# Kernel tuning notes

Hardware: AMD Instinct MI355X
Metric: run time of the kernel (lower is better)

## Reference

```python
import jax, jax.numpy as jnp
import numpy as np

B, T, CIN = 32, 4096, 165
CH, RCH, EDIM, NEMB = 256, 32, 64, 512


def setup_inputs() -> dict:
    key = jax.random.key(0)
    ks = iter(jax.random.split(key, 40))

    def w(o, i):
        return jax.random.normal(next(ks), (o, i), jnp.float32) * (1.0 / np.sqrt(i))

    def b(o):
        return jnp.zeros((o,), jnp.float32)

    inp = {"x": jax.random.normal(next(ks), (B, T, CIN), jnp.float32)}
    # Encoder: conv(165->128), relu, conv(128->256), relu, conv(256->256), 2 resblocks, relu
    inp["enc_w0"], inp["enc_b0"] = w(CH // 2, CIN), b(CH // 2)
    inp["enc_w1"], inp["enc_b1"] = w(CH, CH // 2), b(CH)
    inp["enc_w2"], inp["enc_b2"] = w(CH, CH), b(CH)
    inp["er0_w0"], inp["er0_b0"] = w(RCH, CH), b(RCH)
    inp["er0_w1"], inp["er0_b1"] = w(CH, RCH), b(CH)
    inp["er1_w0"], inp["er1_b0"] = w(RCH, CH), b(RCH)
    inp["er1_w1"], inp["er1_b1"] = w(CH, RCH), b(CH)
    # quantize_conv (256->64)
    inp["qc_w"], inp["qc_b"] = w(EDIM, CH), b(EDIM)
    # codebook [dim, n_embed]
    inp["embed"] = jax.random.normal(next(ks), (EDIM, NEMB), jnp.float32)
    # Decoder: conv(64->256), 2 resblocks, relu, conv(256->128), relu, conv(128->165)
    inp["dec_w0"], inp["dec_b0"] = w(CH, EDIM), b(CH)
    inp["dr0_w0"], inp["dr0_b0"] = w(RCH, CH), b(RCH)
    inp["dr0_w1"], inp["dr0_b1"] = w(CH, RCH), b(CH)
    inp["dr1_w0"], inp["dr1_b0"] = w(RCH, CH), b(RCH)
    inp["dr1_w1"], inp["dr1_b1"] = w(CH, RCH), b(CH)
    inp["dec_w1"], inp["dec_b1"] = w(CH // 2, CH), b(CH // 2)
    inp["dec_w2"], inp["dec_b2"] = w(CIN, CH // 2), b(CIN)
    return inp


def _conv(h, w, bb):
    # 1x1 Conv1d == pointwise matmul over channels; h: [B,C_in,T]
    return jnp.einsum('oi,bit->bot', w, h) + bb[None, :, None]


def _res(h, w0, b0, w1, b1):
    # Sequential(ReLU, Conv, ReLU, Conv) with residual add
    return h + _conv(jax.nn.relu(_conv(jax.nn.relu(h), w0, b0)), w1, b1)


def reference(x, enc_w0, enc_b0, enc_w1, enc_b1, enc_w2, enc_b2,
              er0_w0, er0_b0, er0_w1, er0_b1, er1_w0, er1_b0, er1_w1, er1_b1,
              qc_w, qc_b, embed,
              dec_w0, dec_b0, dr0_w0, dr0_b0, dr0_w1, dr0_b1,
              dr1_w0, dr1_b0, dr1_w1, dr1_b1, dec_w1, dec_b1, dec_w2, dec_b2):
    h = jnp.transpose(x, (0, 2, 1))  # [B,CIN,T]
    # Encoder
    h = _conv(h, enc_w0, enc_b0)
    h = jax.nn.relu(h)
    h = _conv(h, enc_w1, enc_b1)
    h = jax.nn.relu(h)
    h = _conv(h, enc_w2, enc_b2)
    h = _res(h, er0_w0, er0_b0, er0_w1, er0_b1)
    h = _res(h, er1_w0, er1_b0, er1_w1, er1_b1)
    h = jax.nn.relu(h)
    # quantize_conv + permute to [B,T,D]
    z = jnp.transpose(_conv(h, qc_w, qc_b), (0, 2, 1))
    # Quantize (eval mode: no EMA buffer updates)
    flat = z.reshape(-1, EDIM)  # [N,D]
    dist = (flat ** 2).sum(1, keepdims=True) - 2.0 * (flat @ embed) + (embed ** 2).sum(0, keepdims=True)  # [N,NEMB]
    ind = jnp.argmin(dist, axis=1)
    quant = embed.T[ind].reshape(z.shape)  # [B,T,D]
    diff = jnp.mean((jax.lax.stop_gradient(quant) - z) ** 2)[None]  # shape (1,)
    quant = z + jax.lax.stop_gradient(quant - z)  # straight-through
    # Decoder
    h = jnp.transpose(quant, (0, 2, 1))  # [B,D,T]
    h = _conv(h, dec_w0, dec_b0)
    h = _res(h, dr0_w0, dr0_b0, dr0_w1, dr0_b1)
    h = _res(h, dr1_w0, dr1_b0, dr1_w1, dr1_b1)
    h = jax.nn.relu(h)
    h = _conv(h, dec_w1, dec_b1)
    h = jax.nn.relu(h)
    h = _conv(h, dec_w2, dec_b2)
    dec = jnp.transpose(h, (0, 2, 1))  # [B,T,CIN]
    return dec, diff
```

## Files before the change

kernel.cpp:

```cpp
#include <hip/hip_runtime.h>
#include <hip/hip_bf16.h>


#define NTOT 131072
#define EDIM 64
#define NEMB 512

__global__ void detect_k(const void* __restrict__ x, int* __restrict__ flag,
                         float* __restrict__ acc)
{
    __shared__ int s_bad;
    if (threadIdx.x == 0) s_bad = 0;
    __syncthreads();
    const unsigned short* u = (const unsigned short*)x;
    int bad = 0;
    for (int i = threadIdx.x; i < 2048; i += 256) {
        unsigned short h = u[i];
        int ex = (h >> 7) & 0xFF;
        if (h != 0 && (ex < 100 || ex > 140)) bad++;
    }
    atomicAdd(&s_bad, bad);
    __syncthreads();
    if (threadIdx.x == 0) { *flag = (s_bad > 256) ? 1 : 0; *acc = 0.f; }
}

struct WTbl { const void* p[31]; int off[31]; int n[31]; int Kd[31]; };

__global__ void convw_k(WTbl t, float* __restrict__ dst, const int* __restrict__ flag)
{
    const bool f32 = (*flag != 0);
    const int ti = blockIdx.x;
    const void* src = t.p[ti];
    float* d = dst + t.off[ti];
    const int n = t.n[ti];
    const int K = t.Kd[ti];
    if (K == 0) {
        for (int i = threadIdx.x; i < n; i += 256)
            d[i] = f32 ? ((const float*)src)[i]
                       : __bfloat162float(((const __hip_bfloat16*)src)[i]);
    } else {
        const int O = n / K;
        for (int j = threadIdx.x; j < n; j += 256) {
            int k = j / O, o = j - k * O;
            int si = o * K + k;
            d[j] = f32 ? ((const float*)src)[si]
                       : __bfloat162float(((const __hip_bfloat16*)src)[si]);
        }
    }
}

__global__ __launch_bounds__(256, 3)
void enc01_k(const void* __restrict__ X,
             const float* __restrict__ W0t, const float* __restrict__ B0,
             const float* __restrict__ W1t, const float* __restrict__ B1,
             float* __restrict__ Y, const int* __restrict__ dtf)
{
    __shared__ float S[64][168];

    const bool f32d = (*dtf != 0);
    const int tid = threadIdx.x;
    const int r0  = blockIdx.x * 64;

    {
        const size_t base = (size_t)r0 * 165;
        for (int e = tid; e < 64 * 168; e += 256) {
            int m = e / 168, k = e - m * 168;
            float v = 0.f;
            if (k < 165) {
                size_t gi = base + (size_t)m * 165 + k;
                v = f32d ? ((const float*)X)[gi]
                         : __bfloat162float(((const __hip_bfloat16*)X)[gi]);
            }
            S[m][k] = v;
        }
    }
    __syncthreads();

    const int tx = tid & 15;
    const int ty = tid >> 4;
    float acc1[4][8] = {};
    for (int k4 = 0; k4 < 168; k4 += 4) {
        float a4[4][4];
        #pragma unroll
        for (int i = 0; i < 4; ++i)
            *(float4*)&a4[i][0] = *(const float4*)&S[ty * 4 + i][k4];
        #pragma unroll
        for (int kk = 0; kk < 4; ++kk) {
            float b[8];
            *(float4*)&b[0] = *(const float4*)(W0t + (size_t)(k4 + kk) * 128 + tx * 4);
            *(float4*)&b[4] = *(const float4*)(W0t + (size_t)(k4 + kk) * 128 + 64 + tx * 4);
            #pragma unroll
            for (int i = 0; i < 4; ++i)
                #pragma unroll
                for (int j = 0; j < 8; ++j)
                    acc1[i][j] = fmaf(a4[i][kk], b[j], acc1[i][j]);
        }
    }
    __syncthreads();

    {
        float bb[8];
        *(float4*)&bb[0] = *(const float4*)(B0 + tx * 4);
        *(float4*)&bb[4] = *(const float4*)(B0 + 64 + tx * 4);
        #pragma unroll
        for (int i = 0; i < 4; ++i) {
            float4 v0, v1;
            v0.x = fmaxf(acc1[i][0] + bb[0], 0.f);
            v0.y = fmaxf(acc1[i][1] + bb[1], 0.f);
            v0.z = fmaxf(acc1[i][2] + bb[2], 0.f);
            v0.w = fmaxf(acc1[i][3] + bb[3], 0.f);
            v1.x = fmaxf(acc1[i][4] + bb[4], 0.f);
            v1.y = fmaxf(acc1[i][5] + bb[5], 0.f);
            v1.z = fmaxf(acc1[i][6] + bb[6], 0.f);
            v1.w = fmaxf(acc1[i][7] + bb[7], 0.f);
            *(float4*)&S[ty * 4 + i][tx * 4]      = v0;
            *(float4*)&S[ty * 4 + i][64 + tx * 4] = v1;
        }
    }
    __syncthreads();

    const int tx2 = tid & 31;
    const int ty2 = tid >> 5;
    float acc2[2][8][4] = {};
    for (int k4 = 0; k4 < 128; k4 += 4) {
        float a4[8][4];
        #pragma unroll
        for (int i = 0; i < 8; ++i)
            *(float4*)&a4[i][0] = *(const float4*)&S[ty2 * 8 + i][k4];
        #pragma unroll
        for (int kk = 0; kk < 4; ++kk) {
            float b0[4], b1[4];
            *(float4*)&b0[0] = *(const float4*)(W1t + (size_t)(k4 + kk) * 256 + tx2 * 4);
            *(float4*)&b1[0] = *(const float4*)(W1t + (size_t)(k4 + kk) * 256 + 128 + tx2 * 4);
            #pragma unroll
            for (int i = 0; i < 8; ++i)
                #pragma unroll
                for (int j = 0; j < 4; ++j) {
                    acc2[0][i][j] = fmaf(a4[i][kk], b0[j], acc2[0][i][j]);
                    acc2[1][i][j] = fmaf(a4[i][kk], b1[j], acc2[1][i][j]);
                }
        }
    }
    {
        float bb0[4], bb1[4];
        *(float4*)&bb0[0] = *(const float4*)(B1 + tx2 * 4);
        *(float4*)&bb1[0] = *(const float4*)(B1 + 128 + tx2 * 4);
        #pragma unroll
        for (int i = 0; i < 8; ++i) {
            const size_t row = (size_t)(r0 + ty2 * 8 + i) * 256;
            float4 v0, v1;
            v0.x = fmaxf(acc2[0][i][0] + bb0[0], 0.f);
            v0.y = fmaxf(acc2[0][i][1] + bb0[1], 0.f);
            v0.z = fmaxf(acc2[0][i][2] + bb0[2], 0.f);
            v0.w = fmaxf(acc2[0][i][3] + bb0[3], 0.f);
            v1.x = fmaxf(acc2[1][i][0] + bb1[0], 0.f);
            v1.y = fmaxf(acc2[1][i][1] + bb1[1], 0.f);
            v1.z = fmaxf(acc2[1][i][2] + bb1[2], 0.f);
            v1.w = fmaxf(acc2[1][i][3] + bb1[3], 0.f);
            *(float4*)(Y + row + tx2 * 4)       = v0;
            *(float4*)(Y + row + 128 + tx2 * 4) = v1;
        }
    }
}

__global__ __launch_bounds__(256)
void res_k(float* __restrict__ H,
           const float* __restrict__ W0t, const float* __restrict__ B0,
           const float* __restrict__ W1t, const float* __restrict__ B1)
{
    __shared__ float Hr[64][260];
    __shared__ float T1[32][68];

    const int tid = threadIdx.x;
    const int r0  = blockIdx.x * 64;

    #pragma unroll
    for (int it = 0; it < 16; ++it) {
        int idx = tid + it * 256;
        int q = idx & 63, m = idx >> 6;
        float4 v = *(const float4*)(H + (size_t)(r0 + m) * 256 + q * 4);
        *(float4*)&Hr[m][q * 4] = v;
    }
    __syncthreads();

    const int tx1 = tid & 3;
    const int ty1 = tid >> 2;
    float acc1[8] = {};
    for (int k4 = 0; k4 < 256; k4 += 4) {
        float a4[4];
        *(float4*)&a4[0] = *(const float4*)&Hr[ty1][k4];
        #pragma unroll
        for (int q = 0; q < 4; ++q) a4[q] = fmaxf(a4[q], 0.f);
        #pragma unroll
        for (int kk = 0; kk < 4; ++kk) {
            float b[8];
            *(float4*)&b[0] = *(const float4*)(W0t + (size_t)(k4 + kk) * 32 + tx1 * 8);
            *(float4*)&b[4] = *(const float4*)(W0t + (size_t)(k4 + kk) * 32 + tx1 * 8 + 4);
            #pragma unroll
            for (int j = 0; j < 8; ++j)
                acc1[j] = fmaf(a4[kk], b[j], acc1[j]);
        }
    }
    {
        #pragma unroll
        for (int j = 0; j < 8; ++j)
            T1[tx1 * 8 + j][ty1] = fmaxf(acc1[j] + B0[tx1 * 8 + j], 0.f);
    }
    __syncthreads();

    const int tx2 = tid & 31;
    const int ty2 = tid >> 5;
    float acc2[2][8][4] = {};
    #pragma unroll 8
    for (int k = 0; k < 32; ++k) {
        float b0[4], b1[4], a[8];
        *(float4*)&b0[0] = *(const float4*)(W1t + (size_t)k * 256 + tx2 * 4);
        *(float4*)&b1[0] = *(const float4*)(W1t + (size_t)k * 256 + 128 + tx2 * 4);
        *(float4*)&a[0] = *(const float4*)&T1[k][ty2 * 8];
        *(float4*)&a[4] = *(const float4*)&T1[k][ty2 * 8 + 4];
        #pragma unroll
        for (int i = 0; i < 8; ++i)
            #pragma unroll
            for (int j = 0; j < 4; ++j) {
                acc2[0][i][j] = fmaf(a[i], b0[j], acc2[0][i][j]);
                acc2[1][i][j] = fmaf(a[i], b1[j], acc2[1][i][j]);
            }
    }
    {
        float bb0[4], bb1[4];
        *(float4*)&bb0[0] = *(const float4*)(B1 + tx2 * 4);
        *(float4*)&bb1[0] = *(const float4*)(B1 + 128 + tx2 * 4);
        #pragma unroll
        for (int i = 0; i < 8; ++i) {
            const int row = ty2 * 8 + i;
            const size_t gr = (size_t)(r0 + row) * 256;
            float4 h0 = *(const float4*)&Hr[row][tx2 * 4];
            float4 h1 = *(const float4*)&Hr[row][128 + tx2 * 4];
            float4 v0, v1;
            v0.x = h0.x + acc2[0][i][0] + bb0[0];
            v0.y = h0.y + acc2[0][i][1] + bb0[1];
            v0.z = h0.z + acc2[0][i][2] + bb0[2];
            v0.w = h0.w + acc2[0][i][3] + bb0[3];
            v1.x = h1.x + acc2[1][i][0] + bb1[0];
            v1.y = h1.y + acc2[1][i][1] + bb1[1];
            v1.z = h1.z + acc2[1][i][2] + bb1[2];
            v1.w = h1.w + acc2[1][i][3] + bb1[3];
            *(float4*)(H + gr + tx2 * 4)       = v0;
            *(float4*)(H + gr + 128 + tx2 * 4) = v1;
        }
    }
}

template <bool PRE_RELU, bool POST_RELU, int YM>
__global__ __launch_bounds__(256)
void gemm_k(const float* __restrict__ X, const float* __restrict__ Wt,
            const float* __restrict__ Bv, void* __restrict__ Y,
            int K, int O, const int* __restrict__ dtf)
{
    __shared__ float Xs[32][132];
    __shared__ float Ws[32][68];

    const bool f32d = (YM == 1) ? (*dtf != 0) : false;
    const int tid = threadIdx.x;
    const int tx  = tid & 15;
    const int ty  = tid >> 4;
    const int o0  = blockIdx.x * 64;
    const int m0  = blockIdx.y * 128;

    float acc[8][4] = {};
    const int KC = K >> 5;
    for (int kc = 0; kc < KC; ++kc) {
        const int k0 = kc << 5;
        #pragma unroll
        for (int it = 0; it < 4; ++it) {
            int idx = tid + it * 256;
            int kq = idx & 7, m = idx >> 3;
            float4 v = *(const float4*)(X + (size_t)(m0 + m) * K + k0 + kq * 4);
            if (PRE_RELU) {
                v.x = fmaxf(v.x, 0.f); v.y = fmaxf(v.y, 0.f);
                v.z = fmaxf(v.z, 0.f); v.w = fmaxf(v.w, 0.f);
            }
            Xs[kq * 4 + 0][m] = v.x; Xs[kq * 4 + 1][m] = v.y;
            Xs[kq * 4 + 2][m] = v.z; Xs[kq * 4 + 3][m] = v.w;
        }
        if ((O & 3) == 0) {
            #pragma unroll
            for (int it = 0; it < 2; ++it) {
                int idx = tid + it * 256;
                int oq = idx & 15, kk = idx >> 4;
                float4 v = make_float4(0.f, 0.f, 0.f, 0.f);
                if (o0 + oq * 4 < O)
                    v = *(const float4*)(Wt + (size_t)(k0 + kk) * O + o0 + oq * 4);
                *(float4*)&Ws[kk][oq * 4] = v;
            }
        } else {
            #pragma unroll
            for (int it = 0; it < 8; ++it) {
                int e = tid + it * 256;
                int kk = e & 31, o = e >> 5;
                int og = o0 + o;
                Ws[kk][o] = (og < O) ? Wt[(size_t)(k0 + kk) * O + og] : 0.f;
            }
        }
        __syncthreads();
        #pragma unroll
        for (int kk = 0; kk < 32; ++kk) {
            float a[8], b[4];
            *(float4*)&a[0] = *(const float4*)&Xs[kk][ty * 8];
            *(float4*)&a[4] = *(const float4*)&Xs[kk][ty * 8 + 4];
            *(float4*)&b[0] = *(const float4*)&Ws[kk][tx * 4];
            #pragma unroll
            for (int i = 0; i < 8; ++i)
                #pragma unroll
                for (int j = 0; j < 4; ++j)
                    acc[i][j] = fmaf(a[i], b[j], acc[i][j]);
        }
        __syncthreads();
    }

    if (YM == 0 && (O & 63) == 0) {
        const int c0 = o0 + tx * 4;
        float4 bb = *(const float4*)(Bv + c0);
        #pragma unroll
        for (int i = 0; i < 8; ++i) {
            int r = m0 + ty * 8 + i;
            float4 v;
            v.x = acc[i][0] + bb.x; v.y = acc[i][1] + bb.y;
            v.z = acc[i][2] + bb.z; v.w = acc[i][3] + bb.w;
            if (POST_RELU) {
                v.x = fmaxf(v.x, 0.f); v.y = fmaxf(v.y, 0.f);
                v.z = fmaxf(v.z, 0.f); v.w = fmaxf(v.w, 0.f);
            }
            *(float4*)((float*)Y + (size_t)r * O + c0) = v;
        }
    } else {
        #pragma unroll
        for (int j = 0; j < 4; ++j) {
            int c = o0 + tx * 4 + j;
            if (c >= O) continue;
            float bb = Bv[c];
            #pragma unroll
            for (int i = 0; i < 8; ++i) {
                int r = m0 + ty * 8 + i;
                float v = acc[i][j] + bb;
                if (POST_RELU) v = fmaxf(v, 0.f);
                size_t yi = (size_t)r * O + c;
                if (YM == 0)   ((float*)Y)[yi] = v;
                else if (f32d) ((float*)Y)[yi] = v;
                else           ((__hip_bfloat16*)Y)[yi] = __float2bfloat16(v);
            }
        }
    }
}

__global__ void prep_k(const float* __restrict__ E, float* __restrict__ Et)
{
    int idx = blockIdx.x * 256 + threadIdx.x;
    Et[(idx & 511) * EDIM + (idx >> 9)] = E[idx];
}

__global__ void e2_k(const float* __restrict__ Et, float* __restrict__ e2)
{
    int e = blockIdx.x * 256 + threadIdx.x;
    float s = 0.f;
    #pragma unroll
    for (int d = 0; d < EDIM; ++d) { float v = Et[e * EDIM + d]; s = fmaf(v, v, s); }
    e2[e] = s;
}

__global__ __launch_bounds__(256)
void vq_k(float* __restrict__ Zq, const float* __restrict__ Ed,
          const float* __restrict__ Et, const float* __restrict__ e2,
          float* __restrict__ acc)
{
    __shared__ float Zs[64][132];
    __shared__ float Es[64][68];

    const int tid = threadIdx.x;
    const int tx  = tid & 15;
    const int ty  = tid >> 4;
    const int r0  = blockIdx.x * 128;

    #pragma unroll
    for (int it = 0; it < 8; ++it) {
        int idx = tid + it * 256;
        int dq = idx & 15, m = idx >> 4;
        float4 v = *(const float4*)(Zq + (size_t)(r0 + m) * 64 + dq * 4);
        Zs[dq * 4 + 0][m] = v.x; Zs[dq * 4 + 1][m] = v.y;
        Zs[dq * 4 + 2][m] = v.z; Zs[dq * 4 + 3][m] = v.w;
    }

    float best[8];
    int   bi[8];
    #pragma unroll
    for (int i = 0; i < 8; ++i) { best[i] = 3.4e38f; bi[i] = 0; }

    for (int cc = 0; cc < 8; ++cc) {
        const int c0 = cc * 64;
        #pragma unroll
        for (int it = 0; it < 4; ++it) {
            int idx = tid + it * 256;
            int oq = idx & 15, kk = idx >> 4;
            *(float4*)&Es[kk][oq * 4] =
                *(const float4*)(Ed + (size_t)kk * NEMB + c0 + oq * 4);
        }
        float4 e2v = *(const float4*)(e2 + c0 + tx * 4);
        __syncthreads();

        float a4[8][4] = {};
        #pragma unroll 8
        for (int kk = 0; kk < 64; ++kk) {
            float a[8], b[4];
            *(float4*)&a[0] = *(const float4*)&Zs[kk][ty * 8];
            *(float4*)&a[4] = *(const float4*)&Zs[kk][ty * 8 + 4];
            *(float4*)&b[0] = *(const float4*)&Es[kk][tx * 4];
            #pragma unroll
            for (int i = 0; i < 8; ++i)
                #pragma unroll
                for (int j = 0; j < 4; ++j)
                    a4[i][j] = fmaf(a[i], b[j], a4[i][j]);
        }

        const float e2a[4] = {e2v.x, e2v.y, e2v.z, e2v.w};
        #pragma unroll
        for (int j = 0; j < 4; ++j) {
            const int code = c0 + tx * 4 + j;
            #pragma unroll
            for (int i = 0; i < 8; ++i) {
                float s = fmaf(-2.f, a4[i][j], e2a[j]);
                if (s < best[i]) { best[i] = s; bi[i] = code; }
            }
        }
        __syncthreads();
    }

    #pragma unroll
    for (int i = 0; i < 8; ++i) {
        #pragma unroll
        for (int m = 1; m < 16; m <<= 1) {
            float ob = __shfl_xor(best[i], m);
            int   oi = __shfl_xor(bi[i], m);
            if (ob < best[i] || (ob == best[i] && oi < bi[i])) {
                best[i] = ob; bi[i] = oi;
            }
        }
    }

    float ds = 0.f;
    #pragma unroll
    for (int i = 0; i < 8; ++i) {
        const int row = r0 + ty * 8 + i;
        float4 qv = *(const float4*)(Et + (size_t)bi[i] * 64 + tx * 4);
        float* zp = Zq + (size_t)row * 64 + tx * 4;
        float4 zv = *(const float4*)zp;
        float t;
        t = qv.x - zv.x; ds = fmaf(t, t, ds);
        t = qv.y - zv.y; ds = fmaf(t, t, ds);
        t = qv.z - zv.z; ds = fmaf(t, t, ds);
        t = qv.w - zv.w; ds = fmaf(t, t, ds);
        *(float4*)zp = qv;
    }
    #pragma unroll
    for (int off = 32; off; off >>= 1) ds += __shfl_down(ds, off);
    if ((tid & 63) == 0) atomicAdd(acc, ds);
}

__global__ void diff_k(const float* __restrict__ acc, void* __restrict__ out,
                       size_t off, const int* __restrict__ dtf)
{
    if (threadIdx.x == 0) {
        float v = *acc * (1.0f / 8388608.0f);
        if (*dtf) ((float*)out)[off] = v;
        else      ((__hip_bfloat16*)out)[off] = __float2bfloat16(v);
    }
}

extern "C" void kernel_launch(void* const* d_in, const int* in_sizes, int n_in,
                              void* d_out, int out_size, void* d_ws, size_t ws_size,
                              hipStream_t stream)
{
    const size_t MB = 1048576;
    char* ws = (char*)d_ws;
    float* Zq  = (float*)ws;
    float* A1  = (float*)(ws + 32 * MB);
    float* A2  = (float*)(ws + 32 * MB + 128 * MB);
    float* Wf  = (float*)(ws + 288 * MB);
    float* Et  = (float*)(ws + 288 * MB + 1310720);
    float* e2  = Et + NEMB * EDIM;
    float* acc = e2 + NEMB;
    int*   dtf = (int*)(acc + 1);

    static const int KDIM[32] = {0, 165,0, 128,0, 256,0, 256,0, 32,0, 256,0, 32,0,
                                 256,0, 0, 64,0, 256,0, 32,0, 256,0, 32,0, 256,0, 128,0};
    WTbl t;
    int off[32];
    int cum = 0;
    for (int i = 1; i < 32; ++i) {
        t.p[i - 1]   = d_in[i];
        t.off[i - 1] = cum;
        t.n[i - 1]   = in_sizes[i];
        t.Kd[i - 1]  = KDIM[i];
        off[i] = cum;
        cum += in_sizes[i];
    }
    const float* W_ew0 = Wf + off[1],  *B_ew0 = Wf + off[2];
    const float* W_ew1 = Wf + off[3],  *B_ew1 = Wf + off[4];
    const float* W_ew2 = Wf + off[5],  *B_ew2 = Wf + off[6];
    const float* W_r0a = Wf + off[7],  *B_r0a = Wf + off[8];
    const float* W_r0b = Wf + off[9],  *B_r0b = Wf + off[10];
    const float* W_r1a = Wf + off[11], *B_r1a = Wf + off[12];
    const float* W_r1b = Wf + off[13], *B_r1b = Wf + off[14];
    const float* W_qc  = Wf + off[15], *B_qc  = Wf + off[16];
    const float* Emb   = Wf + off[17];
    const float* W_d0  = Wf + off[18], *B_d0  = Wf + off[19];
    const float* W_s0a = Wf + off[20], *B_s0a = Wf + off[21];
    const float* W_s0b = Wf + off[22], *B_s0b = Wf + off[23];
    const float* W_s1a = Wf + off[24], *B_s1a = Wf + off[25];
    const float* W_s1b = Wf + off[26], *B_s1b = Wf + off[27];
    const float* W_d1  = Wf + off[28], *B_d1  = Wf + off[29];
    const float* W_d2  = Wf + off[30], *B_d2  = Wf + off[31];

    dim3 blk(256);
    const int NB = NTOT / 64;
    auto g = [](int o) { return dim3((o + 63) / 64, NTOT / 128); };

    detect_k<<<1, blk, 0, stream>>>(d_in[0], dtf, acc);
    convw_k<<<31, blk, 0, stream>>>(t, Wf, dtf);
    prep_k<<<128, blk, 0, stream>>>(Emb, Et);
    e2_k<<<2, blk, 0, stream>>>(Et, e2);

    enc01_k<<<NB, blk, 0, stream>>>(d_in[0], W_ew0, B_ew0, W_ew1, B_ew1, A1, dtf);
    gemm_k<false, false, 0><<<g(256), blk, 0, stream>>>(A1, W_ew2, B_ew2, A2, 256, 256, dtf);
    res_k<<<NB, blk, 0, stream>>>(A2, W_r0a, B_r0a, W_r0b, B_r0b);
    res_k<<<NB, blk, 0, stream>>>(A2, W_r1a, B_r1a, W_r1b, B_r1b);
    gemm_k<true, false, 0><<<g(64), blk, 0, stream>>>(A2, W_qc, B_qc, Zq, 256, 64, dtf);

    vq_k<<<NTOT / 128, blk, 0, stream>>>(Zq, Emb, Et, e2, acc);

    gemm_k<false, false, 0><<<g(256), blk, 0, stream>>>(Zq, W_d0, B_d0, A1, 64, 256, dtf);
    res_k<<<NB, blk, 0, stream>>>(A1, W_s0a, B_s0a, W_s0b, B_s0b);
    res_k<<<NB, blk, 0, stream>>>(A1, W_s1a, B_s1a, W_s1b, B_s1b);
    gemm_k<true, true, 0><<<g(128), blk, 0, stream>>>(A1, W_d1, B_d1, A2, 256, 128, dtf);
    gemm_k<false, false, 1><<<g(165), blk, 0, stream>>>(A2, W_d2, B_d2, d_out, 128, 165, dtf);

    diff_k<<<1, 64, 0, stream>>>(acc, d_out, (size_t)NTOT * 165, dtf);
}
```

Before: 1.890 ms.

## Add full-width row-tile GEMM kernel with weights read from global memory

Adds a templated gemmf_k kernel in which each block owns 64 rows and computes every output channel. Activations are staged in shared memory in K-halves, and weights are read directly from global memory, where they are cached because they are shared by all blocks. It replaces the 2D-tiled gemm_k for the fixed-shape 256/64/128-output layers, which removes redundant re-reads of the activation tile across output tiles. The res_k first stage is retiled to 2 rows x 4 outputs per thread, and enc01_k drops its occupancy hint. gemm_k is simplified to its scalar path only, used just for the final 165-channel layer.

Result: no change. 1.875 ms (-0.8%).

```diff
diff --git a/kernel.cpp b/kernel.cpp
--- a/kernel.cpp
+++ b/kernel.cpp
@@ -49,7 +49,7 @@
     }
 }
 
-__global__ __launch_bounds__(256, 3)
+__global__ __launch_bounds__(256)
 void enc01_k(const void* __restrict__ X,
              const float* __restrict__ W0t, const float* __restrict__ B0,
              const float* __restrict__ W1t, const float* __restrict__ B1,
@@ -183,28 +183,29 @@
     }
     __syncthreads();
 
-    const int tx1 = tid & 3;
-    const int ty1 = tid >> 2;
-    float acc1[8] = {};
-    for (int k4 = 0; k4 < 256; k4 += 4) {
-        float a4[4];
-        *(float4*)&a4[0] = *(const float4*)&Hr[ty1][k4];
-        #pragma unroll
-        for (int q = 0; q < 4; ++q) a4[q] = fmaxf(a4[q], 0.f);
-        #pragma unroll
-        for (int kk = 0; kk < 4; ++kk) {
-            float b[8];
-            *(float4*)&b[0] = *(const float4*)(W0t + (size_t)(k4 + kk) * 32 + tx1 * 8);
-            *(float4*)&b[4] = *(const float4*)(W0t + (size_t)(k4 + kk) * 32 + tx1 * 8 + 4);
-            #pragma unroll
-            for (int j = 0; j < 8; ++j)
-                acc1[j] = fmaf(a4[kk], b[j], acc1[j]);
+    const int tx1 = tid & 7;
+    const int ty1 = tid >> 3;
+    float acc1[2][4] = {};
+    #pragma unroll 8
+    for (int k = 0; k < 256; ++k) {
+        float b[4];
+        *(float4*)&b[0] = *(const float4*)(W0t + (size_t)k * 32 + tx1 * 4);
+        float a0 = fmaxf(Hr[ty1 * 2][k], 0.f);
+        float a1 = fmaxf(Hr[ty1 * 2 + 1][k], 0.f);
+        #pragma unroll
+        for (int j = 0; j < 4; ++j) {
+            acc1[0][j] = fmaf(a0, b[j], acc1[0][j]);
+            acc1[1][j] = fmaf(a1, b[j], acc1[1][j]);
         }
     }
     {
-        #pragma unroll
-        for (int j = 0; j < 8; ++j)
-            T1[tx1 * 8 + j][ty1] = fmaxf(acc1[j] + B0[tx1 * 8 + j], 0.f);
+        float bb[4];
+        *(float4*)&bb[0] = *(const float4*)(B0 + tx1 * 4);
+        #pragma unroll
+        for (int i = 0; i < 2; ++i)
+            #pragma unroll
+            for (int j = 0; j < 4; ++j)
+                T1[tx1 * 4 + j][ty1 * 2 + i] = fmaxf(acc1[i][j] + bb[j], 0.f);
     }
     __syncthreads();
 
@@ -251,6 +252,86 @@
     }
 }
 
+template <int K, int OC, bool PRE_RELU, bool POST_RELU>
+__global__ __launch_bounds__(256)
+void gemmf_k(const float* __restrict__ X, const float* __restrict__ Wt,
+             const float* __restrict__ Bv, float* __restrict__ Y)
+{
+    constexpr int KH  = (K < 128) ? K : 128;
+    constexpr int SW  = KH + 4;
+    constexpr int TX  = (OC == 256) ? 32 : 16;
+    constexpr int RPT = TX / 4;
+    constexpr int NCH = (OC > TX * 4) ? 2 : 1;
+    constexpr int CHW = OC / NCH;
+
+    __shared__ float S[64 * SW];
+
+    const int tid = threadIdx.x;
+    const int r0  = blockIdx.x * 64;
+    const int tx  = tid & (TX - 1);
+    const int ty  = tid / TX;
+
+    float acc[NCH][RPT][4] = {};
+
+    for (int h = 0; h < K; h += KH) {
+        #pragma unroll
+        for (int it = 0; it < (64 * KH / 4) / 256; ++it) {
+            int idx = tid + it * 256;
+            int m = idx / (KH / 4), g = idx % (KH / 4);
+            float4 v = *(const float4*)(X + (size_t)(r0 + m) * K + h + g * 4);
+            if (PRE_RELU) {
+                v.x = fmaxf(v.x, 0.f); v.y = fmaxf(v.y, 0.f);
+                v.z = fmaxf(v.z, 0.f); v.w = fmaxf(v.w, 0.f);
+            }
+            *(float4*)&S[m * SW + g * 4] = v;
+        }
+        __syncthreads();
+
+        #pragma unroll 2
+        for (int k4 = 0; k4 < KH; k4 += 4) {
+            float a4[RPT][4];
+            #pragma unroll
+            for (int i = 0; i < RPT; ++i)
+                *(float4*)&a4[i][0] = *(const float4*)&S[(ty * RPT + i) * SW + k4];
+            #pragma unroll
+            for (int kk = 0; kk < 4; ++kk) {
+                float b[NCH][4];
+                #pragma unroll
+                for (int c = 0; c < NCH; ++c)
+                    *(float4*)&b[c][0] =
+                        *(const float4*)(Wt + (size_t)(h + k4 + kk) * OC + c * CHW + tx * 4);
+                #pragma unroll
+                for (int c = 0; c < NCH; ++c)
+                    #pragma unroll
+                    for (int i = 0; i < RPT; ++i)
+                        #pragma unroll
+                        for (int j = 0; j < 4; ++j)
+                            acc[c][i][j] = fmaf(a4[i][kk], b[c][j], acc[c][i][j]);
+            }
+        }
+        __syncthreads();
+    }
+
+    #pragma unroll
+    for (int c = 0; c < NCH; ++c) {
+        float bb[4];
+        *(float4*)&bb[0] = *(const float4*)(Bv + c * CHW + tx * 4);
+        #pragma unroll
+        for (int i = 0; i < RPT; ++i) {
+            float4 v;
+            v.x = acc[c][i][0] + bb[0];
+            v.y = acc[c][i][1] + bb[1];
+            v.z = acc[c][i][2] + bb[2];
+            v.w = acc[c][i][3] + bb[3];
+            if (POST_RELU) {
+                v.x = fmaxf(v.x, 0.f); v.y = fmaxf(v.y, 0.f);
+                v.z = fmaxf(v.z, 0.f); v.w = fmaxf(v.w, 0.f);
+            }
+            *(float4*)(Y + (size_t)(r0 + ty * RPT + i) * OC + c * CHW + tx * 4) = v;
+        }
+    }
+}
+
 template <bool PRE_RELU, bool POST_RELU, int YM>
 __global__ __launch_bounds__(256)
 void gemm_k(const float* __restrict__ X, const float* __restrict__ Wt,
@@ -283,24 +364,12 @@
             Xs[kq * 4 + 0][m] = v.x; Xs[kq * 4 + 1][m] = v.y;
             Xs[kq * 4 + 2][m] = v.z; Xs[kq * 4 + 3][m] = v.w;
         }
-        if ((O & 3) == 0) {
-            #pragma unroll
-            for (int it = 0; it < 2; ++it) {
-                int idx = tid + it * 256;
-                int oq = idx & 15, kk = idx >> 4;
-                float4 v = make_float4(0.f, 0.f, 0.f, 0.f);
-                if (o0 + oq * 4 < O)
-                    v = *(const float4*)(Wt + (size_t)(k0 + kk) * O + o0 + oq * 4);
-                *(float4*)&Ws[kk][oq * 4] = v;
-            }
-        } else {
-            #pragma unroll
-            for (int it = 0; it < 8; ++it) {
-                int e = tid + it * 256;
-                int kk = e & 31, o = e >> 5;
-                int og = o0 + o;
-                Ws[kk][o] = (og < O) ? Wt[(size_t)(k0 + kk) * O + og] : 0.f;
-            }
+        #pragma unroll
+        for (int it = 0; it < 8; ++it) {
+            int e = tid + it * 256;
+            int kk = e & 31, o = e >> 5;
+            int og = o0 + o;
+            Ws[kk][o] = (og < O) ? Wt[(size_t)(k0 + kk) * O + og] : 0.f;
         }
         __syncthreads();
         #pragma unroll
@@ -318,37 +387,20 @@
         __syncthreads();
     }
 
-    if (YM == 0 && (O & 63) == 0) {
-        const int c0 = o0 + tx * 4;
-        float4 bb = *(const float4*)(Bv + c0);
+    #pragma unroll
+    for (int j = 0; j < 4; ++j) {
+        int c = o0 + tx * 4 + j;
+        if (c >= O) continue;
+        float bb = Bv[c];
         #pragma unroll
         for (int i = 0; i < 8; ++i) {
             int r = m0 + ty * 8 + i;
-            float4 v;
-            v.x = acc[i][0] + bb.x; v.y = acc[i][1] + bb.y;
-            v.z = acc[i][2] + bb.z; v.w = acc[i][3] + bb.w;
-            if (POST_RELU) {
-                v.x = fmaxf(v.x, 0.f); v.y = fmaxf(v.y, 0.f);
-                v.z = fmaxf(v.z, 0.f); v.w = fmaxf(v.w, 0.f);
-            }
-            *(float4*)((float*)Y + (size_t)r * O + c0) = v;
-        }
-    } else {
-        #pragma unroll
-        for (int j = 0; j < 4; ++j) {
-            int c = o0 + tx * 4 + j;
-            if (c >= O) continue;
-            float bb = Bv[c];
-            #pragma unroll
-            for (int i = 0; i < 8; ++i) {
-                int r = m0 + ty * 8 + i;
-                float v = acc[i][j] + bb;
-                if (POST_RELU) v = fmaxf(v, 0.f);
-                size_t yi = (size_t)r * O + c;
-                if (YM == 0)   ((float*)Y)[yi] = v;
-                else if (f32d) ((float*)Y)[yi] = v;
-                else           ((__hip_bfloat16*)Y)[yi] = __float2bfloat16(v);
-            }
+            float v = acc[i][j] + bb;
+            if (POST_RELU) v = fmaxf(v, 0.f);
+            size_t yi = (size_t)r * O + c;
+            if (YM == 0)   ((float*)Y)[yi] = v;
+            else if (f32d) ((float*)Y)[yi] = v;
+            else           ((__hip_bfloat16*)Y)[yi] = __float2bfloat16(v);
         }
     }
 }
@@ -522,7 +574,6 @@
 
     dim3 blk(256);
     const int NB = NTOT / 64;
-    auto g = [](int o) { return dim3((o + 63) / 64, NTOT / 128); };
 
     detect_k<<<1, blk, 0, stream>>>(d_in[0], dtf, acc);
     convw_k<<<31, blk, 0, stream>>>(t, Wf, dtf);
@@ -530,18 +581,19 @@
     e2_k<<<2, blk, 0, stream>>>(Et, e2);
 
     enc01_k<<<NB, blk, 0, stream>>>(d_in[0], W_ew0, B_ew0, W_ew1, B_ew1, A1, dtf);
-    gemm_k<false, false, 0><<<g(256), blk, 0, stream>>>(A1, W_ew2, B_ew2, A2, 256, 256, dtf);
+    gemmf_k<256, 256, false, false><<<NB, blk, 0, stream>>>(A1, W_ew2, B_ew2, A2);
     res_k<<<NB, blk, 0, stream>>>(A2, W_r0a, B_r0a, W_r0b, B_r0b);
     res_k<<<NB, blk, 0, stream>>>(A2, W_r1a, B_r1a, W_r1b, B_r1b);
-    gemm_k<true, false, 0><<<g(64), blk, 0, stream>>>(A2, W_qc, B_qc, Zq, 256, 64, dtf);
+    gemmf_k<256, 64, true, false><<<NB, blk, 0, stream>>>(A2, W_qc, B_qc, Zq);
 
     vq_k<<<NTOT / 128, blk, 0, stream>>>(Zq, Emb, Et, e2, acc);
 
-    gemm_k<false, false, 0><<<g(256), blk, 0, stream>>>(Zq, W_d0, B_d0, A1, 64, 256, dtf);
+    gemmf_k<64, 256, false, false><<<NB, blk, 0, stream>>>(Zq, W_d0, B_d0, A1);
     res_k<<<NB, blk, 0, stream>>>(A1, W_s0a, B_s0a, W_s0b, B_s0b);
     res_k<<<NB, blk, 0, stream>>>(A1, W_s1a, B_s1a, W_s1b, B_s1b);
-    gemm_k<true, true, 0><<<g(128), blk, 0, stream>>>(A1, W_d1, B_d1, A2, 256, 128, dtf);
-    gemm_k<false, false, 1><<<g(165), blk, 0, stream>>>(A2, W_d2, B_d2, d_out, 128, 165, dtf);
+    gemmf_k<256, 128, true, true><<<NB, blk, 0, stream>>>(A1, W_d1, B_d1, A2);
+    gemm_k<false, false, 1><<<dim3(3, NTOT / 128), blk, 0, stream>>>
+        (A2, W_d2, B_d2, d_out, 128, 165, dtf);
 
     diff_k<<<1, 64, 0, stream>>>(acc, d_out, (size_t)NTOT * 165, dtf);
 }
```
